# Optimization experiments

Hardware: AMD Instinct MI355X
Metric: run time of the kernel (lower is better)

The kernel has to match this reference:

```python
import jax, jax.numpy as jnp
import numpy as np

B, S, D = 8, 2048, 1024

def setup_inputs() -> dict:
    key = jax.random.key(0)
    k1, k2 = jax.random.split(key)
    x = jax.random.normal(k1, (B, S, D), dtype=jnp.float32)
    # nn.Linear(dim, dim, bias=False) weight: [out, in]
    W = jax.random.normal(k2, (D, D), dtype=jnp.float32) * (1.0 / np.sqrt(D))
    return {"x": x, "W": W}

def reference(x, W):
    d = x.shape[-1]
    scale = 1.0 / jnp.sqrt(jnp.float32(d))
    # scores: [B, S, S]
    scores = jnp.einsum('bqd,bkd->bqk', x, x) * scale
    S_len = x.shape[-2]
    causal = jnp.tril(jnp.ones((S_len, S_len), dtype=bool))  # keep lower triangle incl. diag
    scores = jnp.where(causal[None, :, :], scores, -jnp.inf)
    attn_w = jax.nn.softmax(scores, axis=-1)
    attn = jnp.einsum('bqk,bkd->bqd', attn_w, x)
    # nn.Linear: y = attn @ W.T
    return jnp.einsum('bqd,ed->bqe', attn, W)
```

## Files before the change

kernel.cpp:

```cpp
#include <hip/hip_runtime.h>

typedef __attribute__((ext_vector_type(8))) __bf16 bf16x8;
typedef __attribute__((ext_vector_type(4))) float floatx4;

static __device__ __forceinline__ floatx4 mfma16(bf16x8 a, bf16x8 b, floatx4 c) {
  return __builtin_amdgcn_mfma_f32_16x16x32_bf16(a, b, c, 0, 0, 0);
}

static __device__ __forceinline__ unsigned short f2b_bits(float f) {
  __bf16 h = (__bf16)f;
  return __builtin_bit_cast(unsigned short, h);
}

static __device__ __forceinline__ void stage16(const void* g, void* l) {
  __builtin_amdgcn_global_load_lds(
      (__attribute__((address_space(1))) void*)(unsigned long long)g,
      (__attribute__((address_space(3))) void*)(unsigned int)(unsigned long long)l,
      16, 0, 0);
}

#define VM6B() asm volatile("s_waitcnt vmcnt(6)\n\ts_barrier" ::: "memory")
#define VM3B() asm volatile("s_waitcnt vmcnt(3)\n\ts_barrier" ::: "memory")
#define VM0B() asm volatile("s_waitcnt vmcnt(0)\n\ts_barrier" ::: "memory")
#define BAR()  asm volatile("s_barrier" ::: "memory")


__global__ __launch_bounds__(256) void cast_kernel(const float4* __restrict__ x,
                                                   const float4* __restrict__ w,
                                                   uint4* __restrict__ xb,
                                                   uint4* __restrict__ wb,
                                                   float4* __restrict__ lsum) {
  __shared__ unsigned char sl[32768];
  const int st = blockIdx.x, tid = threadIdx.x;
  if (st < 1088) {
    const float4* src = (st < 1024) ? x + (size_t)st * 4096 : w + (size_t)(st - 1024) * 4096;
    uint4* dst = (st < 1024) ? xb + (size_t)st * 2048 : wb + (size_t)(st - 1024) * 2048;
#pragma unroll
    for (int it = 0; it < 16; ++it) {
      const int row = it, c4 = (it * 256 + tid) & 255;
      float4 v = src[row * 256 + c4];
      ushort4 o;
      o.x = f2b_bits(v.x); o.y = f2b_bits(v.y); o.z = f2b_bits(v.z); o.w = f2b_bits(v.w);
      *(ushort4*)(sl + row * 2048 + ((c4 * 8) ^ ((row & 7) << 4))) = o;
    }
    __syncthreads();
#pragma unroll
    for (int it = 0; it < 8; ++it) {
      const int o = it * 4096 + tid * 16;
      const int c = o >> 10, l = (o >> 4) & 63;
      const int row = l & 15, kg = l >> 4;
      uint4 v = *(const uint4*)(sl + row * 2048 + ((c * 64 + kg * 16) ^ ((row & 7) << 4)));
      dst[o >> 4] = v;
    }
  } else {
    const float4 z = {0.0f, 0.0f, 0.0f, 0.0f};
#pragma unroll
    for (int it = 0; it < 4; ++it) lsum[(st - 1088) * 1024 + it * 256 + tid] = z;
  }
}


__global__ __launch_bounds__(512, 2) void zq_fused(const unsigned short* __restrict__ xb,
                                                   const unsigned short* __restrict__ wb,
                                                   unsigned short* __restrict__ zT,
                                                   unsigned short* __restrict__ P,
                                                   float* __restrict__ lsum) {
  extern __shared__ bf16x8 lds[];
  bf16x8* ldsA = lds;
  bf16x8* ldsB = lds + 1536;
  const int tid = threadIdx.x, wid = tid >> 6, lane = tid & 63;
  const int wr = wid >> 2, wc = wid & 3, lr = lane & 15, lq = lane >> 4;
  const int g = blockIdx.x;
  const bool is_qk = (g >= 512);

  const unsigned short* gA;
  const unsigned short* gB0;
  const unsigned short* gB1;
  int b, mt, ntl, rt, ct;
  if (!is_qk) {
    b = g & 7;
    const int gg = g >> 3;
    mt = gg >> 2; ntl = gg & 3;
    gA = xb + ((size_t)b * 4096 + (mt * 8 + wid) * 32) * 512 + lane * 8;
    gB0 = wb + (size_t)((ntl * 16 + wid) * 32) * 512 + lane * 8;
    gB1 = wb + (size_t)((ntl * 16 + wid + 8) * 32) * 512 + lane * 8;
  } else {
    const int h = g - 512;
    b = h & 7;
    const int idx = h >> 3;
    int m = (int)((sqrtf(4.0f * idx + 1.0f) - 1.0f) * 0.5f);
    while ((m + 1) * (m + 2) <= idx) ++m;
    while (m * (m + 1) > idx) --m;
    const int rem = idx - m * (m + 1);
    rt = 2 * m + (rem > m);
    ct = rem - (rem > m ? (m + 1) : 0);
    gA = xb + ((size_t)b * 4096 + (rt * 8 + wid) * 32) * 512 + lane * 8;
    gB0 = xb + ((size_t)b * 4096 + (ct * 16 + wid) * 32) * 512 + lane * 8;
    gB1 = xb + ((size_t)b * 4096 + (ct * 16 + wid + 8) * 32) * 512 + lane * 8;
  }

  floatx4 acc[4][4] = {};

#pragma unroll
  for (int t = 0; t < 2; ++t) {
    stage16(gA + t * 512, &ldsA[t * 512 + wid * 64]);
    stage16(gB0 + t * 512, &ldsB[t * 1024 + wid * 64]);
    stage16(gB1 + t * 512, &ldsB[t * 1024 + (wid + 8) * 64]);
  }

#pragma unroll
  for (int kt = 0; kt < 32; ++kt) {
    const int cb = kt % 3;
    if (kt + 2 < 32) {
      const int sb = (kt + 2) % 3;
      stage16(gA + (kt + 2) * 512, &ldsA[sb * 512 + wid * 64]);
      stage16(gB0 + (kt + 2) * 512, &ldsB[sb * 1024 + wid * 64]);
      stage16(gB1 + (kt + 2) * 512, &ldsB[sb * 1024 + (wid + 8) * 64]);
      VM6B();
    } else if (kt + 1 < 32) {
      VM3B();
    } else {
      VM0B();
    }
    bf16x8 a_[4], b_[4];
#pragma unroll
    for (int i = 0; i < 4; ++i) a_[i] = ldsA[cb * 512 + (wr * 4 + i) * 64 + lane];
#pragma unroll
    for (int j = 0; j < 4; ++j) b_[j] = ldsB[cb * 1024 + (wc * 4 + j) * 64 + lane];
#pragma unroll
    for (int i = 0; i < 4; ++i)
#pragma unroll
      for (int j = 0; j < 4; ++j) acc[i][j] = mfma16(a_[i], b_[j], acc[i][j]);
    BAR();
  }

  if (!is_qk) {
#pragma unroll
    for (int i = 0; i < 4; ++i) {
      const int s0 = mt * 128 + wr * 64 + i * 16 + lq * 4;
      const int s5 = s0 >> 5, s3 = (s0 >> 3) & 3, s7 = s0 & 7;
#pragma unroll
      for (int j = 0; j < 4; ++j) {
        const int e4 = ntl * 16 + wc * 4 + j;
        ushort4 o;
        o.x = f2b_bits(acc[i][j][0]); o.y = f2b_bits(acc[i][j][1]);
        o.z = f2b_bits(acc[i][j][2]); o.w = f2b_bits(acc[i][j][3]);
        *(ushort4*)(zT + ((size_t)b * 4096 + e4 * 64 + s5) * 512 + s3 * 128 + lr * 8 + s7) = o;
      }
    }
  } else {
    const int col128 = 2 * ct + (wc >> 1);
    if (col128 <= rt) {
      const bool diag = (col128 == rt);
      unsigned short* Pt =
          P + ((size_t)b * 136 + (size_t)(rt * (rt + 1) / 2 + col128)) * 16384;
      float* lsb = lsum + b * 2048 + rt * 128;
#pragma unroll
      for (int i = 0; i < 4; ++i) {
        const int row_l = wr * 64 + i * 16 + lq * 4;
        floatx4 rs = {0.0f, 0.0f, 0.0f, 0.0f};
#pragma unroll
        for (int j = 0; j < 4; ++j) {
          const int incol = (wc & 1) * 64 + j * 16 + lr;
          const int cbase = ((wr * 4 + i) * 4 + (wc & 1) * 2 + (j >> 1)) * 512 +
                            ((j * 2 + (lr >> 3)) & 3) * 128 + (lr & 7);
#pragma unroll
          for (int v = 0; v < 4; ++v) {
            float p = __expf(acc[i][j][v] * 0.03125f - 44.0f);
            if (diag && incol > row_l + v) p = 0.0f;
            Pt[cbase + (lq * 4 + v) * 8] = f2b_bits(p);
            rs[v] += p;
          }
        }
#pragma unroll
        for (int v = 0; v < 4; ++v) {
          float s = rs[v];
          s += __shfl_xor(s, 1);
          s += __shfl_xor(s, 2);
          s += __shfl_xor(s, 4);
          s += __shfl_xor(s, 8);
          if (lr == 0) atomicAdd(&lsb[row_l + v], s);
        }
      }
    }
  }
}

__global__ __launch_bounds__(512, 2) void pv_out(const unsigned short* __restrict__ P,
                                                 const unsigned short* __restrict__ zT,
                                                 const float* __restrict__ lsum,
                                                 float* __restrict__ out) {
  extern __shared__ bf16x8 lds[];
  bf16x8* ldsA = lds;
  bf16x8* ldsB = lds + 1536;
  const int tid = threadIdx.x, wid = tid >> 6, lane = tid & 63;
  const int wr = wid >> 2, wc = wid & 3, lr = lane & 15, lq = lane >> 4;
  const int g = blockIdx.x, b = g & 7, gg = g >> 3;
  const int q = gg >> 2;
  const int rt = (gg < 32) ? 15 - q : q - 8;
  const int ntl = gg & 3;
  const int NKT = (rt + 1) * 4;

  const unsigned short* pA =
      P + ((size_t)b * 136 + (size_t)(rt * (rt + 1) / 2)) * 16384 + (size_t)wid * 2048 + lane * 8;
  const unsigned short* gB0 = zT + ((size_t)b * 4096 + (ntl * 16 + wid) * 64) * 512 + lane * 8;
  const unsigned short* gB1 =
      zT + ((size_t)b * 4096 + (ntl * 16 + wid + 8) * 64) * 512 + lane * 8;
  floatx4 acc[4][4] = {};

#pragma unroll
  for (int t = 0; t < 2; ++t) {
    stage16(pA + (t >> 2) * 16384 + (t & 3) * 512, &ldsA[t * 512 + wid * 64]);
    stage16(gB0 + t * 512, &ldsB[t * 1024 + wid * 64]);
    stage16(gB1 + t * 512, &ldsB[t * 1024 + (wid + 8) * 64]);
  }

  int cb = 0, sb = 2;
  for (int kt = 0; kt < NKT; ++kt) {
    if (kt + 2 < NKT) {
      const int k2 = kt + 2;
      stage16(pA + (k2 >> 2) * 16384 + (k2 & 3) * 512, &ldsA[sb * 512 + wid * 64]);
      stage16(gB0 + k2 * 512, &ldsB[sb * 1024 + wid * 64]);
      stage16(gB1 + k2 * 512, &ldsB[sb * 1024 + (wid + 8) * 64]);
      VM6B();
    } else if (kt + 1 < NKT) {
      VM3B();
    } else {
      VM0B();
    }
    bf16x8 a_[4], b_[4];
#pragma unroll
    for (int i = 0; i < 4; ++i) a_[i] = ldsA[cb * 512 + (wr * 4 + i) * 64 + lane];
#pragma unroll
    for (int j = 0; j < 4; ++j) b_[j] = ldsB[cb * 1024 + (wc * 4 + j) * 64 + lane];
#pragma unroll
    for (int i = 0; i < 4; ++i)
#pragma unroll
      for (int j = 0; j < 4; ++j) acc[i][j] = mfma16(a_[i], b_[j], acc[i][j]);
    BAR();
    cb = (cb == 2) ? 0 : cb + 1;
    sb = (sb == 2) ? 0 : sb + 1;
  }

  const float* lsb = lsum + b * 2048 + rt * 128;
  float* outb = out + (size_t)b * 2097152;
#pragma unroll
  for (int i = 0; i < 4; ++i) {
    const int row_l = wr * 64 + i * 16 + lq * 4;
    floatx4 linv;
#pragma unroll
    for (int v = 0; v < 4; ++v) linv[v] = 1.0f / lsb[row_l + v];
#pragma unroll
    for (int j = 0; j < 4; ++j) {
      const int col = ntl * 256 + wc * 64 + j * 16 + lr;
#pragma unroll
      for (int v = 0; v < 4; ++v)
        __builtin_nontemporal_store(acc[i][j][v] * linv[v],
                                    &outb[(size_t)(rt * 128 + row_l + v) * 1024 + col]);
    }
  }
}

extern "C" void kernel_launch(void* const* d_in, const int* in_sizes, int n_in,
                              void* d_out, int out_size, void* d_ws, size_t ws_size,
                              hipStream_t stream) {
  const float* x = (const float*)d_in[0];
  const float* W = (const float*)d_in[1];
  float* out = (float*)d_out;
  char* ws = (char*)d_ws;
  unsigned short* xb = (unsigned short*)ws;
  unsigned short* zT = (unsigned short*)(ws + 33554432ull);
  unsigned short* P  = (unsigned short*)(ws + 67108864ull);
  unsigned short* wb = (unsigned short*)(ws + 67108864ull + 35651584ull + 65536ull);
  float* lsum = (float*)(ws + 67108864ull + 35651584ull);

  static bool attr_done = false;
  if (!attr_done) {
    (void)hipFuncSetAttribute(reinterpret_cast<const void*>(zq_fused),
                              hipFuncAttributeMaxDynamicSharedMemorySize, 73728);
    (void)hipFuncSetAttribute(reinterpret_cast<const void*>(pv_out),
                              hipFuncAttributeMaxDynamicSharedMemorySize, 73728);
    attr_done = true;
  }

  cast_kernel<<<1092, 256, 0, stream>>>((const float4*)x, (const float4*)W,
                                        (uint4*)xb, (uint4*)wb, (float4*)lsum);
  zq_fused<<<1088, 512, 73728, stream>>>(xb, wb, zT, P, lsum);
  pv_out<<<512, 512, 73728, stream>>>(P, zT, lsum, out);
}
```

Measured before the change: 229.5 us.

## Switch GEMM pipelines to double buffering and raise occupancy hint to six

Both GEMM kernels go from a three-stage LDS ring (prefetch distance 2) to a two-stage double buffer (prefetch distance 1), cutting dynamic LDS from 72KB to 48KB. The launch bound's min-blocks hint rises from 2 to 6, which forces the compiler toward a much lower register budget per thread. The aim is more resident workgroups per CU to hide latency. The cost is a shorter prefetch distance and possible register spills of the 4x4 accumulator tile. The cast kernel's column index is also simplified to just tid, which gives the same value as before.

After: 645.2 us. 181% more time.

```diff
diff --git a/kernel.cpp b/kernel.cpp
--- a/kernel.cpp
+++ b/kernel.cpp
@@ -19,7 +19,6 @@
       16, 0, 0);
 }
 
-#define VM6B() asm volatile("s_waitcnt vmcnt(6)\n\ts_barrier" ::: "memory")
 #define VM3B() asm volatile("s_waitcnt vmcnt(3)\n\ts_barrier" ::: "memory")
 #define VM0B() asm volatile("s_waitcnt vmcnt(0)\n\ts_barrier" ::: "memory")
 #define BAR()  asm volatile("s_barrier" ::: "memory")
@@ -37,7 +36,7 @@
     uint4* dst = (st < 1024) ? xb + (size_t)st * 2048 : wb + (size_t)(st - 1024) * 2048;
 #pragma unroll
     for (int it = 0; it < 16; ++it) {
-      const int row = it, c4 = (it * 256 + tid) & 255;
+      const int row = it, c4 = tid;
       float4 v = src[row * 256 + c4];
       ushort4 o;
       o.x = f2b_bits(v.x); o.y = f2b_bits(v.y); o.z = f2b_bits(v.z); o.w = f2b_bits(v.w);
@@ -60,14 +59,14 @@
 }
 
 
-__global__ __launch_bounds__(512, 2) void zq_fused(const unsigned short* __restrict__ xb,
+__global__ __launch_bounds__(512, 6) void zq_fused(const unsigned short* __restrict__ xb,
                                                    const unsigned short* __restrict__ wb,
                                                    unsigned short* __restrict__ zT,
                                                    unsigned short* __restrict__ P,
                                                    float* __restrict__ lsum) {
   extern __shared__ bf16x8 lds[];
   bf16x8* ldsA = lds;
-  bf16x8* ldsB = lds + 1536;
+  bf16x8* ldsB = lds + 1024;
   const int tid = threadIdx.x, wid = tid >> 6, lane = tid & 63;
   const int wr = wid >> 2, wc = wid & 3, lr = lane & 15, lq = lane >> 4;
   const int g = blockIdx.x;
@@ -101,23 +100,18 @@
 
   floatx4 acc[4][4] = {};
 
-#pragma unroll
-  for (int t = 0; t < 2; ++t) {
-    stage16(gA + t * 512, &ldsA[t * 512 + wid * 64]);
-    stage16(gB0 + t * 512, &ldsB[t * 1024 + wid * 64]);
-    stage16(gB1 + t * 512, &ldsB[t * 1024 + (wid + 8) * 64]);
-  }
+  stage16(gA, &ldsA[wid * 64]);
+  stage16(gB0, &ldsB[wid * 64]);
+  stage16(gB1, &ldsB[(wid + 8) * 64]);
 
 #pragma unroll
   for (int kt = 0; kt < 32; ++kt) {
-    const int cb = kt % 3;
-    if (kt + 2 < 32) {
-      const int sb = (kt + 2) % 3;
-      stage16(gA + (kt + 2) * 512, &ldsA[sb * 512 + wid * 64]);
-      stage16(gB0 + (kt + 2) * 512, &ldsB[sb * 1024 + wid * 64]);
-      stage16(gB1 + (kt + 2) * 512, &ldsB[sb * 1024 + (wid + 8) * 64]);
-      VM6B();
-    } else if (kt + 1 < 32) {
+    const int cb = kt & 1;
+    if (kt + 1 < 32) {
+      const int sb = cb ^ 1;
+      stage16(gA + (kt + 1) * 512, &ldsA[sb * 512 + wid * 64]);
+      stage16(gB0 + (kt + 1) * 512, &ldsB[sb * 1024 + wid * 64]);
+      stage16(gB1 + (kt + 1) * 512, &ldsB[sb * 1024 + (wid + 8) * 64]);
       VM3B();
     } else {
       VM0B();
@@ -186,13 +180,13 @@
   }
 }
 
-__global__ __launch_bounds__(512, 2) void pv_out(const unsigned short* __restrict__ P,
+__global__ __launch_bounds__(512, 6) void pv_out(const unsigned short* __restrict__ P,
                                                  const unsigned short* __restrict__ zT,
                                                  const float* __restrict__ lsum,
                                                  float* __restrict__ out) {
   extern __shared__ bf16x8 lds[];
   bf16x8* ldsA = lds;
-  bf16x8* ldsB = lds + 1536;
+  bf16x8* ldsB = lds + 1024;
   const int tid = threadIdx.x, wid = tid >> 6, lane = tid & 63;
   const int wr = wid >> 2, wc = wid & 3, lr = lane & 15, lq = lane >> 4;
   const int g = blockIdx.x, b = g & 7, gg = g >> 3;
@@ -208,22 +202,18 @@
       zT + ((size_t)b * 4096 + (ntl * 16 + wid + 8) * 64) * 512 + lane * 8;
   floatx4 acc[4][4] = {};
 
-#pragma unroll
-  for (int t = 0; t < 2; ++t) {
-    stage16(pA + (t >> 2) * 16384 + (t & 3) * 512, &ldsA[t * 512 + wid * 64]);
-    stage16(gB0 + t * 512, &ldsB[t * 1024 + wid * 64]);
-    stage16(gB1 + t * 512, &ldsB[t * 1024 + (wid + 8) * 64]);
-  }
-
-  int cb = 0, sb = 2;
+  stage16(pA, &ldsA[wid * 64]);
+  stage16(gB0, &ldsB[wid * 64]);
+  stage16(gB1, &ldsB[(wid + 8) * 64]);
+
   for (int kt = 0; kt < NKT; ++kt) {
-    if (kt + 2 < NKT) {
-      const int k2 = kt + 2;
-      stage16(pA + (k2 >> 2) * 16384 + (k2 & 3) * 512, &ldsA[sb * 512 + wid * 64]);
-      stage16(gB0 + k2 * 512, &ldsB[sb * 1024 + wid * 64]);
-      stage16(gB1 + k2 * 512, &ldsB[sb * 1024 + (wid + 8) * 64]);
-      VM6B();
-    } else if (kt + 1 < NKT) {
+    const int cb = kt & 1;
+    if (kt + 1 < NKT) {
+      const int sb = cb ^ 1;
+      const int k1 = kt + 1;
+      stage16(pA + (k1 >> 2) * 16384 + (k1 & 3) * 512, &ldsA[sb * 512 + wid * 64]);
+      stage16(gB0 + k1 * 512, &ldsB[sb * 1024 + wid * 64]);
+      stage16(gB1 + k1 * 512, &ldsB[sb * 1024 + (wid + 8) * 64]);
       VM3B();
     } else {
       VM0B();
@@ -238,8 +228,6 @@
 #pragma unroll
       for (int j = 0; j < 4; ++j) acc[i][j] = mfma16(a_[i], b_[j], acc[i][j]);
     BAR();
-    cb = (cb == 2) ? 0 : cb + 1;
-    sb = (sb == 2) ? 0 : sb + 1;
   }
 
   const float* lsb = lsum + b * 2048 + rt * 128;
@@ -277,14 +265,14 @@
   static bool attr_done = false;
   if (!attr_done) {
     (void)hipFuncSetAttribute(reinterpret_cast<const void*>(zq_fused),
-                              hipFuncAttributeMaxDynamicSharedMemorySize, 73728);
+                              hipFuncAttributeMaxDynamicSharedMemorySize, 49152);
     (void)hipFuncSetAttribute(reinterpret_cast<const void*>(pv_out),
-                              hipFuncAttributeMaxDynamicSharedMemorySize, 73728);
+                              hipFuncAttributeMaxDynamicSharedMemorySize, 49152);
     attr_done = true;
   }
 
   cast_kernel<<<1092, 256, 0, stream>>>((const float4*)x, (const float4*)W,
                                         (uint4*)xb, (uint4*)wb, (float4*)lsum);
-  zq_fused<<<1088, 512, 73728, stream>>>(xb, wb, zT, P, lsum);
-  pv_out<<<512, 512, 73728, stream>>>(P, zT, lsum, out);
-}
+  zq_fused<<<1088, 512, 49152, stream>>>(xb, wb, zT, P, lsum);
+  pv_out<<<512, 512, 49152, stream>>>(P, zT, lsum, out);
+}
```
